# Optimization experiments

Measured on AMD Instinct MI355X. Metric: run time of the kernel, lower is better.

Reference implementation:

```python
import jax, jax.numpy as jnp
import numpy as np

N_NODES = 100000
N_EDGES = 600000
IN_C, HID, OUT_C = 128, 256, 1

def _glorot(key, shape):
    fan_in, fan_out = shape[1], shape[0]
    lim = np.sqrt(6.0 / (fan_in + fan_out))
    return jax.random.uniform(key, shape, jnp.float32, -lim, lim)

def setup_inputs() -> dict:
    key = jax.random.key(0)
    ks = jax.random.split(key, 12)
    x = jax.random.normal(ks[0], (N_NODES, IN_C), jnp.float32)
    edge_index = jax.random.randint(ks[1], (2, N_EDGES), 0, N_NODES, jnp.int32)
    return {
        "x": x,
        "edge_index": edge_index,
        # SAGEConv1: lin_l (neighbors, with bias), lin_r (root, no bias)
        "W1l": _glorot(ks[2], (HID, IN_C)),
        "b1": jnp.zeros((HID,), jnp.float32),
        "W1r": _glorot(ks[3], (HID, IN_C)),
        # SAGEConv2
        "W2l": _glorot(ks[4], (HID, HID)),
        "b2": jnp.zeros((HID,), jnp.float32),
        "W2r": _glorot(ks[5], (HID, HID)),
        # MLP head: Linear(HID, HID//2) -> ReLU -> Linear(HID//2, OUT_C)
        "Wf1": _glorot(ks[6], (HID // 2, HID)),
        "bf1": jnp.zeros((HID // 2,), jnp.float32),
        "Wf2": _glorot(ks[7], (OUT_C, HID // 2)),
        "bf2": jnp.zeros((OUT_C,), jnp.float32),
    }

def _sage_conv(x, src, dst, Wl, b, Wr, n_nodes):
    # mean-aggregate source-node features into destination nodes
    msgs = x[src]  # [E, F] gather
    sums = jax.ops.segment_sum(msgs, dst, num_segments=n_nodes)
    cnt = jax.ops.segment_sum(jnp.ones((src.shape[0], 1), x.dtype), dst,
                              num_segments=n_nodes)
    mean = sums / jnp.maximum(cnt, 1.0)  # isolated nodes -> 0
    return mean @ Wl.T + b + x @ Wr.T

def reference(x, edge_index, W1l, b1, W1r, W2l, b2, W2r, Wf1, bf1, Wf2, bf2):
    src, dst = edge_index[0], edge_index[1]
    n = x.shape[0]
    h = jax.nn.elu(_sage_conv(x, src, dst, W1l, b1, W1r, n))
    # dropout p=0.3 is identity in eval mode
    h = jax.nn.elu(_sage_conv(h, src, dst, W2l, b2, W2r, n))
    h = jax.nn.relu(h @ Wf1.T + bf1)
    out = h @ Wf2.T + bf2  # [N, 1]
    return jnp.squeeze(out)
```

## Files before the change

### kernel.cpp

```cpp
#include <hip/hip_runtime.h>
#include <hip/hip_bf16.h>

#define NN 100000
#define NE 600000
#define NBLK 98
#define MPAD 100096

typedef __attribute__((ext_vector_type(4))) int   i32x4;
typedef __attribute__((ext_vector_type(4))) float f32x4;

__device__ __forceinline__ float b2f(unsigned short u) {
  unsigned int v = ((unsigned int)u) << 16;
  return __uint_as_float(v);
}
__device__ __forceinline__ unsigned short f2b(float f) {
  __hip_bfloat16 h = __float2bfloat16(f);
  return *reinterpret_cast<unsigned short*>(&h);
}
__device__ __forceinline__ float elu(float v) {
  return v > 0.0f ? v : (expf(v) - 1.0f);
}
__device__ __forceinline__ void gload_lds16(const void* g, void* l) {
  __builtin_amdgcn_global_load_lds(
      (const __attribute__((address_space(1))) void*)g,
      (__attribute__((address_space(3))) void*)l, 16, 0, 0);
}
__device__ __forceinline__ f32x4 mfma16(i32x4 a, i32x4 b, f32x4 c) {
  asm volatile("v_mfma_f32_16x16x32_bf16 %0, %1, %2, %0"
               : "+v"(c) : "v"(a), "v"(b));
  return c;
}

__global__ __launch_bounds__(256) void hist_kernel(
    const int* __restrict__ ei, int* __restrict__ deg) {
  const int* dst = ei + NE;
  int i = blockIdx.x * 256 + threadIdx.x;
  int n = gridDim.x * 256;
  for (int e = i; e < NE; e += n) atomicAdd(&deg[dst[e]], 1);
}

__global__ __launch_bounds__(256) void scan1_kernel(
    const int* __restrict__ deg, int* __restrict__ row, int* __restrict__ aux) {
  __shared__ int sd[256];
  int b = blockIdx.x, t = threadIdx.x;
  int base = b * 1024 + t * 4;
  int v0 = (base + 0 < NN) ? deg[base + 0] : 0;
  int v1 = (base + 1 < NN) ? deg[base + 1] : 0;
  int v2 = (base + 2 < NN) ? deg[base + 2] : 0;
  int v3 = (base + 3 < NN) ? deg[base + 3] : 0;
  int s = v0 + v1 + v2 + v3;
  sd[t] = s;
  __syncthreads();
  for (int off = 1; off < 256; off <<= 1) {
    int tmp = (t >= off) ? sd[t - off] : 0;
    __syncthreads();
    sd[t] += tmp;
    __syncthreads();
  }
  int excl = sd[t] - s;
  if (base + 0 < NN) row[base + 0] = excl;
  if (base + 1 < NN) row[base + 1] = excl + v0;
  if (base + 2 < NN) row[base + 2] = excl + v0 + v1;
  if (base + 3 < NN) row[base + 3] = excl + v0 + v1 + v2;
  if (t == 255) aux[b] = sd[t];
}

__global__ __launch_bounds__(256) void scan2_kernel(int* __restrict__ aux) {
  __shared__ int sd[256];
  int t = threadIdx.x;
  int v = (t < NBLK) ? aux[t] : 0;
  sd[t] = v;
  __syncthreads();
  for (int off = 1; off < 256; off <<= 1) {
    int tmp = (t >= off) ? sd[t - off] : 0;
    __syncthreads();
    sd[t] += tmp;
    __syncthreads();
  }
  if (t < NBLK) aux[t] = sd[t] - v;
}

__global__ __launch_bounds__(256) void scan3_kernel(
    int* __restrict__ row, const int* __restrict__ aux) {
  int i = blockIdx.x * 256 + threadIdx.x;
  if (i < NN) row[i] += aux[i >> 10];
  if (i == 0) row[NN] = NE;
}

__global__ __launch_bounds__(256) void fill_kernel(
    const int* __restrict__ ei, const int* __restrict__ row,
    int* __restrict__ cur, int* __restrict__ eidx) {
  const int* src = ei;
  const int* dst = ei + NE;
  int i = blockIdx.x * 256 + threadIdx.x;
  int n = gridDim.x * 256;
  for (int e = i; e < NE; e += n) {
    int d = dst[e];
    int p = atomicAdd(&cur[d], 1);
    eidx[row[d] + p] = src[e];
  }
}

__global__ __launch_bounds__(256) void conv_x(
    const float* __restrict__ x, unsigned short* __restrict__ A1) {
  int i = blockIdx.x * 256 + threadIdx.x;
  if (i >= NN * 32) return;
  int n = i >> 5, k4 = i & 31;
  float4 v = ((const float4*)(x + (size_t)n * 128))[k4];
  ushort4 o;
  o.x = f2b(v.x); o.y = f2b(v.y); o.z = f2b(v.z); o.w = f2b(v.w);
  ((ushort4*)(A1 + (size_t)n * 256 + 128))[k4] = o;
}

__global__ __launch_bounds__(256) void conv_w(
    const float* __restrict__ W1l, const float* __restrict__ W1r,
    const float* __restrict__ W2l, const float* __restrict__ W2r,
    const float* __restrict__ Wf1,
    unsigned short* __restrict__ W1b, unsigned short* __restrict__ W2b,
    unsigned short* __restrict__ Wf1b) {
  int i = blockIdx.x * 256 + threadIdx.x;
  const float* srcp;
  unsigned short* dstp;
  if (i < 16384) {
    int e = i * 4, j = e >> 8, k = e & 255;
    srcp = (k < 128) ? (W1l + (size_t)j * 128 + k) : (W1r + (size_t)j * 128 + (k - 128));
    dstp = W1b + e;
  } else if (i < 49152) {
    int e = (i - 16384) * 4, j = e >> 9, k = e & 511;
    srcp = (k < 256) ? (W2l + (size_t)j * 256 + k) : (W2r + (size_t)j * 256 + (k - 256));
    dstp = W2b + e;
  } else if (i < 57344) {
    int e = (i - 49152) * 4;
    srcp = Wf1 + e;
    dstp = Wf1b + e;
  } else return;
  float4 v = *(const float4*)srcp;
  ushort4 o;
  o.x = f2b(v.x); o.y = f2b(v.y); o.z = f2b(v.z); o.w = f2b(v.w);
  *(ushort4*)dstp = o;
}

__global__ __launch_bounds__(256) void agg1_csr(
    unsigned short* __restrict__ A1, const int* __restrict__ row,
    const int* __restrict__ eidx) {
  int lane = threadIdx.x & 63;
  int n = (blockIdx.x * 256 + threadIdx.x) >> 6;
  if (n >= NN) return;
  int r0 = row[n], r1 = row[n + 1];
  float ax = 0.f, ay = 0.f;
  int e = r0;
  for (; e + 3 < r1; e += 4) {
    int s0 = eidx[e], s1 = eidx[e + 1], s2 = eidx[e + 2], s3 = eidx[e + 3];
    ushort2 a = ((const ushort2*)(A1 + (size_t)s0 * 256 + 128))[lane];
    ushort2 b = ((const ushort2*)(A1 + (size_t)s1 * 256 + 128))[lane];
    ushort2 c = ((const ushort2*)(A1 + (size_t)s2 * 256 + 128))[lane];
    ushort2 d = ((const ushort2*)(A1 + (size_t)s3 * 256 + 128))[lane];
    ax += (b2f(a.x) + b2f(b.x)) + (b2f(c.x) + b2f(d.x));
    ay += (b2f(a.y) + b2f(b.y)) + (b2f(c.y) + b2f(d.y));
  }
  for (; e < r1; ++e) {
    int s0 = eidx[e];
    ushort2 a = ((const ushort2*)(A1 + (size_t)s0 * 256 + 128))[lane];
    ax += b2f(a.x);
    ay += b2f(a.y);
  }
  float inv = 1.0f / (float)max(r1 - r0, 1);
  ushort2 o;
  o.x = f2b(ax * inv);
  o.y = f2b(ay * inv);
  ((ushort2*)(A1 + (size_t)n * 256))[lane] = o;
}

__global__ __launch_bounds__(256) void agg2_csr(
    unsigned short* __restrict__ A2, const int* __restrict__ row,
    const int* __restrict__ eidx) {
  int lane = threadIdx.x & 63;
  int n = (blockIdx.x * 256 + threadIdx.x) >> 6;
  if (n >= NN) return;
  int r0 = row[n], r1 = row[n + 1];
  float4 acc = make_float4(0.f, 0.f, 0.f, 0.f);
  int e = r0;
  for (; e + 3 < r1; e += 4) {
    int s0 = eidx[e], s1 = eidx[e + 1], s2 = eidx[e + 2], s3 = eidx[e + 3];
    ushort4 a = ((const ushort4*)(A2 + (size_t)s0 * 512 + 256))[lane];
    ushort4 b = ((const ushort4*)(A2 + (size_t)s1 * 512 + 256))[lane];
    ushort4 c = ((const ushort4*)(A2 + (size_t)s2 * 512 + 256))[lane];
    ushort4 d = ((const ushort4*)(A2 + (size_t)s3 * 512 + 256))[lane];
    acc.x += (b2f(a.x) + b2f(b.x)) + (b2f(c.x) + b2f(d.x));
    acc.y += (b2f(a.y) + b2f(b.y)) + (b2f(c.y) + b2f(d.y));
    acc.z += (b2f(a.z) + b2f(b.z)) + (b2f(c.z) + b2f(d.z));
    acc.w += (b2f(a.w) + b2f(b.w)) + (b2f(c.w) + b2f(d.w));
  }
  for (; e < r1; ++e) {
    int s0 = eidx[e];
    ushort4 a = ((const ushort4*)(A2 + (size_t)s0 * 512 + 256))[lane];
    acc.x += b2f(a.x);
    acc.y += b2f(a.y);
    acc.z += b2f(a.z);
    acc.w += b2f(a.w);
  }
  float inv = 1.0f / (float)max(r1 - r0, 1);
  ushort4 o;
  o.x = f2b(acc.x * inv);
  o.y = f2b(acc.y * inv);
  o.z = f2b(acc.z * inv);
  o.w = f2b(acc.w * inv);
  ((ushort4*)(A2 + (size_t)n * 512))[lane] = o;
}

template <int K, int APITCH, int EPI>
__global__ __launch_bounds__(256, 4) void gemm_kernel(
    const unsigned short* __restrict__ A, const unsigned short* __restrict__ Wb,
    const float* __restrict__ bias, const float* __restrict__ w2,
    const float* __restrict__ bf2p,
    unsigned short* __restrict__ Hout, int HPITCH, int HOFF,
    float* __restrict__ out) {
  __shared__ unsigned short lA[2][4096];
  __shared__ unsigned short lB[2][4096];
  int tid = threadIdx.x;
  int w = tid >> 6, lane = tid & 63;
  int lhi = lane >> 4, llo = lane & 15;
  int m0 = blockIdx.x * 128;
  int c0 = blockIdx.y * 128;
  int fb = lane * 8;

  f32x4 acc0[8], acc1[8];
#pragma unroll
  for (int n = 0; n < 8; ++n) { acc0[n] = (f32x4)0.f; acc1[n] = (f32x4)0.f; }

#define STAGE(t)                                                                \
  do {                                                                          \
    int _b = (t) & 1;                                                           \
    int _k0 = (t) * 32;                                                         \
    _Pragma("unroll")                                                           \
    for (int i = 0; i < 2; ++i) {                                               \
      int c = w * 2 + i;                                                        \
      const unsigned short* ga =                                                \
          A + (size_t)(m0 + c * 16 + llo) * APITCH + _k0 + lhi * 8;             \
      gload_lds16(ga, &lA[_b][c * 512]);                                        \
      const unsigned short* gb =                                                \
          Wb + (size_t)(c0 + c * 16 + llo) * K + _k0 + lhi * 8;                 \
      gload_lds16(gb, &lB[_b][c * 512]);                                        \
    }                                                                           \
  } while (0)

  constexpr int NSTEP = K / 32;
  STAGE(0);
  __builtin_amdgcn_sched_barrier(0);
  asm volatile("s_waitcnt vmcnt(0)" ::: "memory");
  __syncthreads();
  for (int t = 0; t < NSTEP; ++t) {
    if (t + 1 < NSTEP) STAGE(t + 1);
    const unsigned short* la = &lA[t & 1][0];
    const unsigned short* lb = &lB[t & 1][0];
    i32x4 a0 = *(const i32x4*)(la + (w * 2 + 0) * 512 + fb);
    i32x4 a1 = *(const i32x4*)(la + (w * 2 + 1) * 512 + fb);
#pragma unroll
    for (int n = 0; n < 8; ++n) {
      i32x4 b = *(const i32x4*)(lb + n * 512 + fb);
      acc0[n] = mfma16(a0, b, acc0[n]);
      acc1[n] = mfma16(a1, b, acc1[n]);
    }
    __builtin_amdgcn_sched_barrier(0);
    asm volatile("s_waitcnt vmcnt(0)" ::: "memory");
    __syncthreads();
  }
#undef STAGE
  asm volatile("s_nop 7\n\ts_nop 7");

  if constexpr (EPI == 0) {
    float bv[8];
#pragma unroll
    for (int n = 0; n < 8; ++n) bv[n] = bias[c0 + n * 16 + llo];
#pragma unroll
    for (int mi = 0; mi < 2; ++mi) {
#pragma unroll
      for (int n = 0; n < 8; ++n) {
        f32x4 av = mi ? acc1[n] : acc0[n];
#pragma unroll
        for (int r = 0; r < 4; ++r) {
          int R = m0 + (w * 2 + mi) * 16 + lhi * 4 + r;
          float v = elu(av[r] + bv[n]);
          Hout[(size_t)R * HPITCH + HOFF + c0 + n * 16 + llo] = f2b(v);
        }
      }
    }
  } else {
    float b1v[8], w2v[8];
#pragma unroll
    for (int n = 0; n < 8; ++n) {
      b1v[n] = bias[n * 16 + llo];
      w2v[n] = w2[n * 16 + llo];
    }
    float bf2v = bf2p[0];
#pragma unroll
    for (int mi = 0; mi < 2; ++mi) {
#pragma unroll
      for (int r = 0; r < 4; ++r) {
        float s = 0.f;
#pragma unroll
        for (int n = 0; n < 8; ++n) {
          f32x4 av = mi ? acc1[n] : acc0[n];
          s += fmaxf(av[r] + b1v[n], 0.f) * w2v[n];
        }
        s += __shfl_xor(s, 1);
        s += __shfl_xor(s, 2);
        s += __shfl_xor(s, 4);
        s += __shfl_xor(s, 8);
        int R = m0 + (w * 2 + mi) * 16 + lhi * 4 + r;
        if (llo == 0 && R < NN) out[R] = s + bf2v;
      }
    }
  }
}

extern "C" void kernel_launch(void* const* d_in, const int* in_sizes, int n_in,
                              void* d_out, int out_size, void* d_ws, size_t ws_size,
                              hipStream_t stream) {
  const float* x   = (const float*)d_in[0];
  const int*   ei  = (const int*)d_in[1];
  const float* W1l = (const float*)d_in[2];
  const float* b1  = (const float*)d_in[3];
  const float* W1r = (const float*)d_in[4];
  const float* W2l = (const float*)d_in[5];
  const float* b2  = (const float*)d_in[6];
  const float* W2r = (const float*)d_in[7];
  const float* Wf1 = (const float*)d_in[8];
  const float* bf1 = (const float*)d_in[9];
  const float* Wf2 = (const float*)d_in[10];
  const float* bf2 = (const float*)d_in[11];
  float* out = (float*)d_out;

  char* ws = (char*)d_ws;
  size_t o = 0;
  int* deg = (int*)(ws + o); o += 400384;
  int* cur = (int*)(ws + o); o += 400384;
  size_t zero_bytes = o;
  int* row  = (int*)(ws + o); o += 400640;
  int* aux  = (int*)(ws + o); o += 4096;
  int* eidx = (int*)(ws + o); o += 2400000;
  unsigned short* A1 = (unsigned short*)(ws + o); o += (size_t)MPAD * 256 * 2;
  unsigned short* A2 = (unsigned short*)(ws + o); o += (size_t)MPAD * 512 * 2;
  unsigned short* h2 = (unsigned short*)(ws + o); o += (size_t)MPAD * 256 * 2;
  unsigned short* W1b  = (unsigned short*)(ws + o); o += 131072;
  unsigned short* W2b  = (unsigned short*)(ws + o); o += 262144;
  unsigned short* Wf1b = (unsigned short*)(ws + o); o += 65536;

  hipMemsetAsync(d_ws, 0, zero_bytes, stream);

  hist_kernel<<<2048, 256, 0, stream>>>(ei, deg);
  scan1_kernel<<<NBLK, 256, 0, stream>>>(deg, row, aux);
  scan2_kernel<<<1, 256, 0, stream>>>(aux);
  scan3_kernel<<<(NN + 255) / 256, 256, 0, stream>>>(row, aux);
  fill_kernel<<<2048, 256, 0, stream>>>(ei, row, cur, eidx);

  conv_x<<<(NN * 32 + 255) / 256, 256, 0, stream>>>(x, A1);
  conv_w<<<224, 256, 0, stream>>>(W1l, W1r, W2l, W2r, Wf1, W1b, W2b, Wf1b);

  agg1_csr<<<25000, 256, 0, stream>>>(A1, row, eidx);
  gemm_kernel<256, 256, 0><<<dim3(MPAD / 128, 2), 256, 0, stream>>>(
      A1, W1b, b1, nullptr, nullptr, A2, 512, 256, nullptr);
  agg2_csr<<<25000, 256, 0, stream>>>(A2, row, eidx);
  gemm_kernel<512, 512, 0><<<dim3(MPAD / 128, 2), 256, 0, stream>>>(
      A2, W2b, b2, nullptr, nullptr, h2, 256, 0, nullptr);
  gemm_kernel<256, 256, 1><<<dim3(MPAD / 128, 1), 256, 0, stream>>>(
      h2, Wf1b, bf1, Wf2, bf2, nullptr, 0, 0, out);
}
```

Baseline: 307.4 us.

## Pre-pack weights and h2 into MFMA tile layout for contiguous LDS loads

Weights are converted into a tile-major bf16 layout in which each 16x32 fragment is contiguous. GEMM B loads then read consecutive 16-byte chunks per lane instead of strided rows. The second conv GEMM writes h2 directly in that packed tile layout, so the head GEMM's A loads are also contiguous. The cost is scattered 2-byte stores in the packed epilogue, which coalesce less well than the row-major writes did.

```diff
diff --git a/kernel.cpp b/kernel.cpp
--- a/kernel.cpp
+++ b/kernel.cpp
@@ -30,6 +30,7 @@
                : "+v"(c) : "v"(a), "v"(b));
   return c;
 }
+
 
 __global__ __launch_bounds__(256) void hist_kernel(
     const int* __restrict__ ei, int* __restrict__ deg) {
@@ -118,26 +119,29 @@
     const float* __restrict__ Wf1,
     unsigned short* __restrict__ W1b, unsigned short* __restrict__ W2b,
     unsigned short* __restrict__ Wf1b) {
-  int i = blockIdx.x * 256 + threadIdx.x;
-  const float* srcp;
-  unsigned short* dstp;
-  if (i < 16384) {
-    int e = i * 4, j = e >> 8, k = e & 255;
-    srcp = (k < 128) ? (W1l + (size_t)j * 128 + k) : (W1r + (size_t)j * 128 + (k - 128));
-    dstp = W1b + e;
-  } else if (i < 49152) {
-    int e = (i - 16384) * 4, j = e >> 9, k = e & 511;
-    srcp = (k < 256) ? (W2l + (size_t)j * 256 + k) : (W2r + (size_t)j * 256 + (k - 256));
-    dstp = W2b + e;
-  } else if (i < 57344) {
-    int e = (i - 49152) * 4;
-    srcp = Wf1 + e;
-    dstp = Wf1b + e;
+  int g = blockIdx.x * 256 + threadIdx.x;
+  const float* src;
+  unsigned short* dst;
+  int j, k, NC;
+  if (g < 8192) {
+    j = g >> 5; k = (g & 31) * 8; NC = 256; dst = W1b;
+    src = (k < 128) ? (W1l + (size_t)j * 128 + k)
+                    : (W1r + (size_t)j * 128 + (k - 128));
+  } else if (g < 24576) {
+    int h = g - 8192; j = h >> 6; k = (h & 63) * 8; NC = 256; dst = W2b;
+    src = (k < 256) ? (W2l + (size_t)j * 256 + k)
+                    : (W2r + (size_t)j * 256 + (k - 256));
+  } else if (g < 28672) {
+    int h = g - 24576; j = h >> 5; k = (h & 31) * 8; NC = 128; dst = Wf1b;
+    src = Wf1 + (size_t)j * 256 + k;
   } else return;
-  float4 v = *(const float4*)srcp;
-  ushort4 o;
-  o.x = f2b(v.x); o.y = f2b(v.y); o.z = f2b(v.z); o.w = f2b(v.w);
-  *(ushort4*)dstp = o;
+  float4 v0 = *(const float4*)src;
+  float4 v1 = *(const float4*)(src + 4);
+  unsigned short o[8] = {f2b(v0.x), f2b(v0.y), f2b(v0.z), f2b(v0.w),
+                         f2b(v1.x), f2b(v1.y), f2b(v1.z), f2b(v1.w)};
+  size_t off = (size_t)(k >> 5) * (NC * 32) + (j >> 4) * 512 +
+               ((k >> 3) & 3) * 128 + (j & 15) * 8;
+  *(i32x4*)(dst + off) = *(i32x4*)o;
 }
 
 __global__ __launch_bounds__(256) void agg1_csr(
@@ -208,7 +212,7 @@
   ((ushort4*)(A2 + (size_t)n * 512))[lane] = o;
 }
 
-template <int K, int APITCH, int EPI>
+template <int K, int APITCH, int EPI, int AP, int BNC, int HPACK>
 __global__ __launch_bounds__(256, 4) void gemm_kernel(
     const unsigned short* __restrict__ A, const unsigned short* __restrict__ Wb,
     const float* __restrict__ bias, const float* __restrict__ w2,
@@ -231,15 +235,19 @@
 #define STAGE(t)                                                                \
   do {                                                                          \
     int _b = (t) & 1;                                                           \
-    int _k0 = (t) * 32;                                                         \
     _Pragma("unroll")                                                           \
     for (int i = 0; i < 2; ++i) {                                               \
       int c = w * 2 + i;                                                        \
-      const unsigned short* ga =                                                \
-          A + (size_t)(m0 + c * 16 + llo) * APITCH + _k0 + lhi * 8;             \
+      const unsigned short* ga;                                                 \
+      if constexpr (AP) {                                                       \
+        ga = A + (size_t)(m0 >> 7) * (128 * K) + (size_t)(t) * 4096 +           \
+             c * 512 + lane * 8;                                                \
+      } else {                                                                  \
+        ga = A + (size_t)(m0 + c * 16 + llo) * APITCH + (t) * 32 + lhi * 8;     \
+      }                                                                         \
       gload_lds16(ga, &lA[_b][c * 512]);                                        \
-      const unsigned short* gb =                                                \
-          Wb + (size_t)(c0 + c * 16 + llo) * K + _k0 + lhi * 8;                 \
+      const unsigned short* gb = Wb + (size_t)(t) * (BNC * 32) +                \
+                                 ((c0 >> 4) + c) * 512 + lane * 8;              \
       gload_lds16(gb, &lB[_b][c * 512]);                                        \
     }                                                                           \
   } while (0)
@@ -281,7 +289,15 @@
         for (int r = 0; r < 4; ++r) {
           int R = m0 + (w * 2 + mi) * 16 + lhi * 4 + r;
           float v = elu(av[r] + bv[n]);
-          Hout[(size_t)R * HPITCH + HOFF + c0 + n * 16 + llo] = f2b(v);
+          if constexpr (HPACK) {
+            int col = c0 + n * 16 + llo;
+            size_t off = (size_t)(R >> 7) * 32768 + (col >> 5) * 4096 +
+                         ((R >> 4) & 7) * 512 + ((col >> 3) & 3) * 128 +
+                         (R & 15) * 8 + (col & 7);
+            Hout[off] = f2b(v);
+          } else {
+            Hout[(size_t)R * HPITCH + HOFF + c0 + n * 16 + llo] = f2b(v);
+          }
         }
       }
     }
@@ -355,14 +371,14 @@
   fill_kernel<<<2048, 256, 0, stream>>>(ei, row, cur, eidx);
 
   conv_x<<<(NN * 32 + 255) / 256, 256, 0, stream>>>(x, A1);
-  conv_w<<<224, 256, 0, stream>>>(W1l, W1r, W2l, W2r, Wf1, W1b, W2b, Wf1b);
+  conv_w<<<112, 256, 0, stream>>>(W1l, W1r, W2l, W2r, Wf1, W1b, W2b, Wf1b);
 
   agg1_csr<<<25000, 256, 0, stream>>>(A1, row, eidx);
-  gemm_kernel<256, 256, 0><<<dim3(MPAD / 128, 2), 256, 0, stream>>>(
+  gemm_kernel<256, 256, 0, 0, 256, 0><<<dim3(MPAD / 128, 2), 256, 0, stream>>>(
       A1, W1b, b1, nullptr, nullptr, A2, 512, 256, nullptr);
   agg2_csr<<<25000, 256, 0, stream>>>(A2, row, eidx);
-  gemm_kernel<512, 512, 0><<<dim3(MPAD / 128, 2), 256, 0, stream>>>(
-      A2, W2b, b2, nullptr, nullptr, h2, 256, 0, nullptr);
-  gemm_kernel<256, 256, 1><<<dim3(MPAD / 128, 1), 256, 0, stream>>>(
+  gemm_kernel<512, 512, 0, 0, 256, 1><<<dim3(MPAD / 128, 2), 256, 0, stream>>>(
+      A2, W2b, b2, nullptr, nullptr, h2, 0, 0, nullptr);
+  gemm_kernel<256, 256, 1, 1, 128, 0><<<dim3(MPAD / 128, 1), 256, 0, stream>>>(
       h2, Wf1b, bf1, Wf2, bf2, nullptr, 0, 0, out);
 }
```

New measurement: 286.0 us. 7.0% less time.
